# Performance work log

Measured on AMD Instinct MI355X. Metric: run time of the kernel, lower is better.

The kernel has to match this reference:

```python
import jax, jax.numpy as jnp
import numpy as np

H, C = 8, 32          # heads, out_channels per head (H*C = 256)
D = H * C
NEG_SLOPE = 0.2
SELF_LOOP_TYPE = 6    # num_edge_types - 1
EPS_LN = 1e-5
EPS_BN = 1e-5


def _gat_layer(x, src, dst, ea, et, Ws, Wd, a_s, a_d, We, ae, te, Wo, bo, b, lg, lb):
    N = x.shape[0]
    xs = (x @ Ws).reshape(N, H, C)   # lin_src -> x_j features
    xd = (x @ Wd).reshape(N, H, C)   # lin_dst -> x_i features
    # per-node attention logits (gathered per edge): alpha = <x_i, att_src> + <x_j, att_dst>
    a_i = jnp.einsum('nhc,hc->nh', xd, a_s)  # paired with x_i (dst)
    a_j = jnp.einsum('nhc,hc->nh', xs, a_d)  # paired with x_j (src)
    alpha = a_i[dst] + a_j[src]                                  # [E, H]
    ef = (ea @ We).reshape(-1, H, C)                              # lin_edge
    alpha = alpha + jnp.einsum('ehc,hc->eh', ef, ae)
    tf = te[et].reshape(-1, H, C)                                 # edge_type_emb
    alpha = alpha + jnp.einsum('ehc,hc->eh', tf, ae)
    alpha = jnp.where(alpha >= 0, alpha, NEG_SLOPE * alpha)       # leaky_relu
    # segment softmax over destination nodes (every node has a self loop)
    m = jax.ops.segment_max(alpha, dst, num_segments=N)
    e = jnp.exp(alpha - m[dst])
    s = jax.ops.segment_sum(e, dst, num_segments=N)
    alpha = e / (s[dst] + 1e-16)                                  # [E, H]
    # dropout is identity in eval mode
    msg = xs[src] * alpha[:, :, None]                             # [E, H, C]
    out = jax.ops.segment_sum(msg, dst, num_segments=N).reshape(N, D)
    out = out @ Wo + bo + b                                       # lin_out + bias
    mu = out.mean(-1, keepdims=True)
    var = out.var(-1, keepdims=True)
    out = (out - mu) / jnp.sqrt(var + EPS_LN) * lg + lb           # layer norm
    return out + x                                                # in_channels == H*C residual


def _bn_relu(x, g, bvec, relu=True):
    mu = x.mean(0)
    var = x.var(0)
    x = (x - mu) / jnp.sqrt(var + EPS_BN) * g + bvec
    return jnp.maximum(x, 0.0) if relu else x


def _forward(x, edge_index, edge_attr, edge_types,
             Ws1, Wd1, as1, ad1, We1, ae1, te1, Wo1, bo1, b1, lg1, lb1,
             Ws2, Wd2, as2, ad2, We2, ae2, te2, Wo2, bo2, b2, lg2, lb2,
             bng1, bnb1, bng2, bnb2):
    N = x.shape[0]
    loops = jnp.arange(N, dtype=edge_index.dtype)
    src = jnp.concatenate([edge_index[0], loops])
    dst = jnp.concatenate([edge_index[1], loops])
    ea = jnp.concatenate([edge_attr, jnp.ones((N, edge_attr.shape[1]), edge_attr.dtype)])
    et = jnp.concatenate([edge_types, jnp.full((N,), SELF_LOOP_TYPE, edge_types.dtype)])
    residual = x  # in_channels == out_channels -> identity projection
    out = _gat_layer(x, src, dst, ea, et, Ws1, Wd1, as1, ad1, We1, ae1, te1, Wo1, bo1, b1, lg1, lb1)
    out = _bn_relu(out, bng1, bnb1, relu=True)   # dropout identity in eval
    out = _gat_layer(out, src, dst, ea, et, Ws2, Wd2, as2, ad2, We2, ae2, te2, Wo2, bo2, b2, lg2, lb2)
    out = _bn_relu(out, bng2, bnb2, relu=False)
    return jnp.maximum(out + residual, 0.0)


def setup_inputs() -> dict:
    key = jax.random.key(0)
    ks = jax.random.split(key, 32)
    N, E, EDIM, NTYPES = 20000, 320000, 16, 7
    d = {}
    d['x'] = jax.random.normal(ks[0], (N, D), jnp.float32)
    d['edge_index'] = jax.random.randint(ks[1], (2, E), 0, N, jnp.int64)
    d['edge_attr'] = jax.random.normal(ks[2], (E, EDIM), jnp.float32)
    d['edge_types'] = jax.random.randint(ks[3], (E,), 0, NTYPES, jnp.int64)
    def glorot(k, shape):
        fan = shape[-2] + shape[-1] if len(shape) >= 2 else shape[-1] + 1
        return jax.random.uniform(k, shape, jnp.float32, -1.0, 1.0) * np.sqrt(6.0 / fan)
    i = 4
    for L in ('1', '2'):
        d['Ws' + L] = glorot(ks[i], (D, D)); i += 1
        d['Wd' + L] = glorot(ks[i], (D, D)); i += 1
        d['as' + L] = glorot(ks[i], (H, C)); i += 1
        d['ad' + L] = glorot(ks[i], (H, C)); i += 1
        d['We' + L] = glorot(ks[i], (EDIM, D)); i += 1
        d['ae' + L] = glorot(ks[i], (H, C)); i += 1
        d['te' + L] = glorot(ks[i], (NTYPES, D)); i += 1
        d['Wo' + L] = glorot(ks[i], (D, D)); i += 1
        d['bo' + L] = jnp.zeros((D,), jnp.float32)
        d['b' + L] = jnp.zeros((D,), jnp.float32)
        d['lg' + L] = jnp.ones((D,), jnp.float32)
        d['lb' + L] = jnp.zeros((D,), jnp.float32)
    d['bng1'] = jnp.ones((D,), jnp.float32); d['bnb1'] = jnp.zeros((D,), jnp.float32)
    d['bng2'] = jnp.ones((D,), jnp.float32); d['bnb2'] = jnp.zeros((D,), jnp.float32)
    return d


def reference(x, edge_index, edge_attr, edge_types,
              Ws1, Wd1, as1, ad1, We1, ae1, te1, Wo1, bo1, b1, lg1, lb1,
              Ws2, Wd2, as2, ad2, We2, ae2, te2, Wo2, bo2, b2, lg2, lb2,
              bng1, bnb1, bng2, bnb2):
    return _forward(x, edge_index, edge_attr, edge_types,
                    Ws1, Wd1, as1, ad1, We1, ae1, te1, Wo1, bo1, b1, lg1, lb1,
                    Ws2, Wd2, as2, ad2, We2, ae2, te2, Wo2, bo2, b2, lg2, lb2,
                    bng1, bnb1, bng2, bnb2)
```

## Files before the change

kernel.cpp:

```cpp
#include <hip/hip_runtime.h>

#define DD 256
#define HH 8
#define CC 32
#define DCACHE 128

typedef __attribute__((ext_vector_type(8))) short short8;
typedef __attribute__((ext_vector_type(4))) float f32x4;

static __device__ __forceinline__ unsigned short f2b(float f){
  unsigned u = __float_as_uint(f);
  u = u + 0x7FFFu + ((u >> 16) & 1u);
  return (unsigned short)(u >> 16);
}
static __device__ __forceinline__ float b2f(unsigned short s){
  return __uint_as_float(((unsigned)s) << 16);
}

static __device__ __forceinline__ void gload16(const void* g, void* l){
  using gpt = const __attribute__((address_space(1))) unsigned int*;
  using lpt = __attribute__((address_space(3))) unsigned int*;
  __builtin_amdgcn_global_load_lds((gpt)(unsigned long long)g, (lpt)(unsigned long long)l, 16, 0, 0);
}

__global__ void k_zero_i(int* p, int n){ int i=blockIdx.x*blockDim.x+threadIdx.x; if(i<n) p[i]=0; }

__global__ void k_count(const int* __restrict__ dstE, int E, int N, int* cnt){
  int e=blockIdx.x*blockDim.x+threadIdx.x;
  if(e<E+N){ int d=(e<E)? dstE[e] : (e-E); atomicAdd(&cnt[d],1); }
}

__global__ __launch_bounds__(1024) void k_scan(const int* __restrict__ cnt, int N, int* row_off, int* cursor){
  __shared__ int part[1024];
  int t=threadIdx.x;
  int chunk=(N+1023)>>10;
  int s=0;
  for(int j=0;j<chunk;j++){ int i=t*chunk+j; if(i<N) s+=cnt[i]; }
  part[t]=s; __syncthreads();
  for(int off=1; off<1024; off<<=1){
    int v=(t>=off)? part[t-off]:0;
    __syncthreads();
    part[t]+=v;
    __syncthreads();
  }
  int run=(t==0)?0:part[t-1];
  for(int j=0;j<chunk;j++){ int i=t*chunk+j; if(i<N){ row_off[i]=run; cursor[i]=run; run+=cnt[i]; } }
  if(t==1023) row_off[N]=part[1023];
}

__global__ void k_fill(const int* __restrict__ srcE, const int* __restrict__ dstE,
                       const float* __restrict__ ea, const int* __restrict__ et,
                       int E, int N, int* cursor,
                       int* esrc, int* etP, float* eaP){
  int e=blockIdx.x*blockDim.x+threadIdx.x;
  if(e>=E+N) return;
  int s,d,ty;
  float4 q0,q1,q2,q3;
  if(e<E){
    s=srcE[e]; d=dstE[e]; ty=et[e];
    q0=*(const float4*)&ea[(size_t)e*16+0];
    q1=*(const float4*)&ea[(size_t)e*16+4];
    q2=*(const float4*)&ea[(size_t)e*16+8];
    q3=*(const float4*)&ea[(size_t)e*16+12];
  }else{
    s=e-E; d=s; ty=6;
    q0=q1=q2=q3=make_float4(1.f,1.f,1.f,1.f);
  }
  int pos=atomicAdd(&cursor[d],1);
  esrc[pos]=s; etP[pos]=ty;
  float* o=&eaP[(size_t)pos*16];
  *(float4*)(o+0)=q0; *(float4*)(o+4)=q1; *(float4*)(o+8)=q2; *(float4*)(o+12)=q3;
}

__global__ void k_cvt_wT4(const float* __restrict__ W0, const float* __restrict__ W1,
                          const float* __restrict__ W2, const float* __restrict__ W3,
                          unsigned short* __restrict__ T0, unsigned short* __restrict__ T1,
                          unsigned short* __restrict__ T2, unsigned short* __restrict__ T3){
  int m=blockIdx.y, c=blockIdx.x, k=threadIdx.x;
  const float* W = (m==0)?W0:(m==1)?W1:(m==2)?W2:W3;
  unsigned short* T = (m==0)?T0:(m==1)?T1:(m==2)?T2:T3;
  T[(size_t)c*DD+k] = f2b(W[(size_t)k*DD+c]);
}

__global__ void k_pre2(const float* __restrict__ Wd1, const float* __restrict__ as1,
                       const float* __restrict__ We1, const float* __restrict__ ae1,
                       const float* __restrict__ te1,
                       const float* __restrict__ Wd2, const float* __restrict__ as2,
                       const float* __restrict__ We2, const float* __restrict__ ae2,
                       const float* __restrict__ te2,
                       float* wd_as1, float* v_e1, float* t_a1,
                       float* wd_as2, float* v_e2, float* t_a2){
  int L=blockIdx.x;
  const float* Wd=L?Wd2:Wd1; const float* as_=L?as2:as1;
  const float* We=L?We2:We1; const float* ae=L?ae2:ae1; const float* te=L?te2:te1;
  float* wd_as=L?wd_as2:wd_as1; float* v_e=L?v_e2:v_e1; float* t_a=L?t_a2:t_a1;
  int t=threadIdx.x;
  for(int idx=t; idx<DD*HH; idx+=256){
    int k=idx>>3, h=idx&7;
    const float* w=&Wd[k*DD+h*CC]; const float* a=&as_[h*CC];
    float s=0;
    #pragma unroll
    for(int c=0;c<CC;c++) s+=w[c]*a[c];
    wd_as[idx]=s;
  }
  for(int idx=t; idx<16*HH; idx+=256){
    int k=idx>>3, h=idx&7;
    const float* w=&We[k*DD+h*CC]; const float* a=&ae[h*CC];
    float s=0;
    #pragma unroll
    for(int c=0;c<CC;c++) s+=w[c]*a[c];
    v_e[idx]=s;
  }
  for(int idx=t; idx<7*HH; idx+=256){
    int k=idx>>3, h=idx&7;
    const float* w=&te[k*DD+h*CC]; const float* a=&ae[h*CC];
    float s=0;
    #pragma unroll
    for(int c=0;c<CC;c++) s+=w[c]*a[c];
    t_a[idx]=s;
  }
}

#define NB_BA 1024
__global__ __launch_bounds__(256) void k_cvt_x2(const float* __restrict__ xin, const float* __restrict__ wd_as,
                         unsigned short* __restrict__ xb, float* __restrict__ a_i, int N){
  int b=blockIdx.x, tid=threadIdx.x, wv=tid>>6, l=tid&63;
  int c0=4*l;
  float wa[4][8];
  #pragma unroll
  for(int j=0;j<4;j++)
    #pragma unroll
    for(int h=0;h<8;h++) wa[j][h]=wd_as[(c0+j)*8+h];
  for(int n=b*4+wv; n<N; n+=NB_BA*4){
    float4 v=*(const float4*)&xin[(size_t)n*DD+c0];
    ushort4 xo; xo.x=f2b(v.x); xo.y=f2b(v.y); xo.z=f2b(v.z); xo.w=f2b(v.w);
    *(ushort4*)&xb[(size_t)n*DD+c0]=xo;
    float ai[8];
    #pragma unroll
    for(int h=0;h<8;h++) ai[h]=v.x*wa[0][h]+v.y*wa[1][h]+v.z*wa[2][h]+v.w*wa[3][h];
    #pragma unroll
    for(int off=1;off<64;off<<=1){
      #pragma unroll
      for(int h=0;h<8;h++) ai[h]+=__shfl_xor(ai[h],off);
    }
    if(l==0){
      float4 A; A.x=ai[0];A.y=ai[1];A.z=ai[2];A.w=ai[3];
      float4 B; B.x=ai[4];B.y=ai[5];B.z=ai[6];B.w=ai[7];
      *(float4*)&a_i[(size_t)n*HH]=A;
      *(float4*)&a_i[(size_t)n*HH+4]=B;
    }
  }
}

template<bool AJ>
__global__ __launch_bounds__(256) void k_gemm1(const unsigned short* __restrict__ A,
                                               const unsigned short* __restrict__ Bt,
                                               const float* __restrict__ ad, float* __restrict__ a_j,
                                               unsigned short* __restrict__ Cout, int N){
  __shared__ char lds[2*12288];
  int tid=threadIdx.x;
  int w=tid>>6, l=tid&63;
  int row0=blockIdx.y*64, col0=blockIdx.x*128;

  int lr=l>>2;
  int kc=(l&3)^((l>>3)&3);
  const unsigned short* ga  = &A [(size_t)(row0+16*w+lr)*DD + kc*8];
  const unsigned short* gb0 = &Bt[(size_t)(col0+32*w+lr)*DD + kc*8];
  const unsigned short* gb1 = &Bt[(size_t)(col0+32*w+16+lr)*DD + kc*8];
  int laoff =      w*1024;
  int lboff0=4096+(32*w)*64;
  int lboff1=4096+(32*w+16)*64;

  int x15=l&15;
  int lp=x15*64 + ((l>>4)^((x15>>1)&3))*16;

  f32x4 acc[4][2];
  #pragma unroll
  for(int i=0;i<4;i++){ acc[i][0]=(f32x4)0.f; acc[i][1]=(f32x4)0.f; }

  gload16(ga,  lds+laoff);
  gload16(gb0, lds+lboff0);
  gload16(gb1, lds+lboff1);
  __syncthreads();
  int cur=0;
  for(int kt=0;kt<DD;kt+=32){
    int nxt=cur^1;
    if(kt+32<DD){
      gload16(ga +kt+32, lds+nxt*12288+laoff);
      gload16(gb0+kt+32, lds+nxt*12288+lboff0);
      gload16(gb1+kt+32, lds+nxt*12288+lboff1);
    }
    char* base=lds+cur*12288;
    short8 af[4], bf[2];
    #pragma unroll
    for(int mf=0;mf<4;mf++) af[mf]=*(short8*)(base + mf*1024 + lp);
    #pragma unroll
    for(int nf=0;nf<2;nf++) bf[nf]=*(short8*)(base + 4096 + (32*w+16*nf)*64 + lp);
    #pragma unroll
    for(int mf=0;mf<4;mf++)
      #pragma unroll
      for(int nf=0;nf<2;nf++)
        acc[mf][nf]=__builtin_amdgcn_mfma_f32_16x16x32_bf16(af[mf],bf[nf],acc[mf][nf],0,0,0);
    __syncthreads();
    cur=nxt;
  }

  int lcol=x15, lrow4=(l>>4)*4;
  float ad0=0.f, ad1=0.f;
  if(AJ){ ad0=ad[col0+32*w+lcol]; ad1=ad[col0+32*w+16+lcol]; }
  int head=(col0>>5)+w;
  #pragma unroll
  for(int mf=0;mf<4;mf++){
    #pragma unroll
    for(int nf=0;nf<2;nf++){
      int col=col0 + 32*w + 16*nf + lcol;
      #pragma unroll
      for(int rr=0;rr<4;rr++){
        int row=row0 + 16*mf + lrow4 + rr;
        if(row<N) Cout[(size_t)row*DD+col]=f2b(acc[mf][nf][rr]);
      }
    }
    if(AJ){
      #pragma unroll
      for(int rr=0;rr<4;rr++){
        float t=acc[mf][0][rr]*ad0 + acc[mf][1][rr]*ad1;
        t+=__shfl_xor(t,1); t+=__shfl_xor(t,2);
        t+=__shfl_xor(t,4); t+=__shfl_xor(t,8);
        int row=row0 + 16*mf + lrow4 + rr;
        if(x15==0 && row<N) a_j[(size_t)row*HH+head]=t;
      }
    }
  }
}

__global__ __launch_bounds__(256) void k_gemm_ln(const unsigned short* __restrict__ A,
                                                 const unsigned short* __restrict__ Bt,
                                                 const float* __restrict__ bo, const float* __restrict__ bvec,
                                                 const float* __restrict__ xin,
                                                 const float* __restrict__ lg, const float* __restrict__ lb,
                                                 float* __restrict__ hout,
                                                 float* __restrict__ psum, float* __restrict__ psq, int N){
  __shared__ char lds[2*18432];
  int tid=threadIdx.x;
  int w=tid>>6, l=tid&63;
  int row0=blockIdx.x*32;

  int lr=l>>2;
  int kc=(l&3)^((l>>3)&3);
  const unsigned short* ga = &A[(size_t)(row0+16*w+lr)*DD + kc*8];
  const unsigned short* gb0=&Bt[(size_t)(64*w   +lr)*DD + kc*8];
  const unsigned short* gb1=&Bt[(size_t)(64*w+16+lr)*DD + kc*8];
  const unsigned short* gb2=&Bt[(size_t)(64*w+32+lr)*DD + kc*8];
  const unsigned short* gb3=&Bt[(size_t)(64*w+48+lr)*DD + kc*8];
  int laoff =      w*1024;
  int lboff0=2048+(64*w   )*64;
  int lboff1=2048+(64*w+16)*64;
  int lboff2=2048+(64*w+32)*64;
  int lboff3=2048+(64*w+48)*64;

  int x15=l&15;
  int lp=x15*64 + ((l>>4)^((x15>>1)&3))*16;

  f32x4 acc[2][4];
  #pragma unroll
  for(int i=0;i<2;i++)
    #pragma unroll
    for(int j=0;j<4;j++) acc[i][j]=(f32x4)0.f;

  if(w<2) gload16(ga, lds+laoff);
  gload16(gb0, lds+lboff0);
  gload16(gb1, lds+lboff1);
  gload16(gb2, lds+lboff2);
  gload16(gb3, lds+lboff3);
  __syncthreads();
  int cur=0;
  for(int kt=0;kt<DD;kt+=32){
    int nxt=cur^1;
    if(kt+32<DD){
      char* nb=lds+nxt*18432;
      if(w<2) gload16(ga+kt+32, nb+laoff);
      gload16(gb0+kt+32, nb+lboff0);
      gload16(gb1+kt+32, nb+lboff1);
      gload16(gb2+kt+32, nb+lboff2);
      gload16(gb3+kt+32, nb+lboff3);
    }
    char* base=lds+cur*18432;
    short8 af[2], bf[4];
    #pragma unroll
    for(int mf=0;mf<2;mf++) af[mf]=*(short8*)(base + mf*1024 + lp);
    #pragma unroll
    for(int nf=0;nf<4;nf++) bf[nf]=*(short8*)(base + 2048 + (64*w+16*nf)*64 + lp);
    #pragma unroll
    for(int mf=0;mf<2;mf++)
      #pragma unroll
      for(int nf=0;nf<4;nf++)
        acc[mf][nf]=__builtin_amdgcn_mfma_f32_16x16x32_bf16(af[mf],bf[nf],acc[mf][nf],0,0,0);
    __syncthreads();
    cur=nxt;
  }

  int lrow4=(l>>4)*4;
  float lgv[4], lbv[4];
  #pragma unroll
  for(int nf=0;nf<4;nf++){
    int col=64*w+16*nf+x15;
    float badd=bo[col]+bvec[col];
    lgv[nf]=lg[col]; lbv[nf]=lb[col];
    #pragma unroll
    for(int mf=0;mf<2;mf++)
      #pragma unroll
      for(int rr=0;rr<4;rr++) acc[mf][nf][rr]+=badd;
  }
  __syncthreads();
  float* rs   =(float*)lds;
  float* rq   =(float*)(lds+512);
  float* mus  =(float*)(lds+1024);
  float* rstds=(float*)(lds+1152);
  #pragma unroll
  for(int mf=0;mf<2;mf++){
    #pragma unroll
    for(int rr=0;rr<4;rr++){
      float t=acc[mf][0][rr]+acc[mf][1][rr]+acc[mf][2][rr]+acc[mf][3][rr];
      float q=acc[mf][0][rr]*acc[mf][0][rr]+acc[mf][1][rr]*acc[mf][1][rr]
             +acc[mf][2][rr]*acc[mf][2][rr]+acc[mf][3][rr]*acc[mf][3][rr];
      t+=__shfl_xor(t,1); q+=__shfl_xor(q,1);
      t+=__shfl_xor(t,2); q+=__shfl_xor(q,2);
      t+=__shfl_xor(t,4); q+=__shfl_xor(q,4);
      t+=__shfl_xor(t,8); q+=__shfl_xor(q,8);
      if(x15==0){
        int row=16*mf+lrow4+rr;
        rs[w*32+row]=t; rq[w*32+row]=q;
      }
    }
  }
  __syncthreads();
  if(tid<32){
    float S=rs[tid]+rs[32+tid]+rs[64+tid]+rs[96+tid];
    float Q=rq[tid]+rq[32+tid]+rq[64+tid]+rq[96+tid];
    float mu=S*(1.f/DD);
    float var=Q*(1.f/DD)-mu*mu;
    mus[tid]=mu;
    rstds[tid]=rsqrtf(var+1e-5f);
  }
  __syncthreads();
  float cps[4]={0.f,0.f,0.f,0.f}, cqs[4]={0.f,0.f,0.f,0.f};
  #pragma unroll
  for(int mf=0;mf<2;mf++){
    #pragma unroll
    for(int rr=0;rr<4;rr++){
      int row=16*mf+lrow4+rr;
      int grow=row0+row;
      bool ok=(grow<N);
      float mu=mus[row], rstd=rstds[row];
      #pragma unroll
      for(int nf=0;nf<4;nf++){
        int col=64*w+16*nf+x15;
        float h=0.f;
        if(ok){
          h=(acc[mf][nf][rr]-mu)*rstd*lgv[nf]+lbv[nf]+xin[(size_t)grow*DD+col];
          hout[(size_t)grow*DD+col]=h;
        }
        cps[nf]+=h; cqs[nf]+=h*h;
      }
    }
  }
  #pragma unroll
  for(int nf=0;nf<4;nf++){
    cps[nf]+=__shfl_xor(cps[nf],16); cqs[nf]+=__shfl_xor(cqs[nf],16);
    cps[nf]+=__shfl_xor(cps[nf],32); cqs[nf]+=__shfl_xor(cqs[nf],32);
  }
  if(l<16){
    #pragma unroll
    for(int nf=0;nf<4;nf++){
      int col=64*w+16*nf+l;
      psum[(size_t)blockIdx.x*DD+col]=cps[nf];
      psq [(size_t)blockIdx.x*DD+col]=cqs[nf];
    }
  }
}

__global__ __launch_bounds__(256) void k_agg(const int* __restrict__ row_off,
                      const int* __restrict__ esrc, const int* __restrict__ etP,
                      const float* __restrict__ eaP,
                      const float* __restrict__ a_i, const float* __restrict__ a_j,
                      const float* __restrict__ v_e, const float* __restrict__ t_a,
                      const unsigned short* __restrict__ ysb, unsigned short* __restrict__ aggb, int N){
  __shared__ float cache[4][DCACHE][8];
  __shared__ int   scache[4][DCACHE];
  int wv=threadIdx.x>>6, l=threadIdx.x&63;
  int n=blockIdx.x*4+wv;
  if(n>=N) return;
  int beg=row_off[n], deg=row_off[n+1]-beg;
  int slotL=l>>3, headL=l&7;
  float veh[16];
  #pragma unroll
  for(int k=0;k<16;k++) veh[k]=v_e[k*8+headL];
  float aih=a_i[(size_t)n*HH+headL];
  float mx=-3e38f;
  for(int i=slotL;i<deg;i+=8){
    size_t pos=(size_t)(beg+i);
    int src=esrc[pos];
    int ty=etP[pos];
    float aj=a_j[(size_t)src*HH+headL];
    const float* eap=&eaP[pos*16];
    float4 q0=*(const float4*)(eap+0);
    float4 q1=*(const float4*)(eap+4);
    float4 q2=*(const float4*)(eap+8);
    float4 q3=*(const float4*)(eap+12);
    float v=aih+aj+t_a[ty*8+headL];
    v+=q0.x*veh[0]+q0.y*veh[1]+q0.z*veh[2]+q0.w*veh[3];
    v+=q1.x*veh[4]+q1.y*veh[5]+q1.z*veh[6]+q1.w*veh[7];
    v+=q2.x*veh[8]+q2.y*veh[9]+q2.z*veh[10]+q2.w*veh[11];
    v+=q3.x*veh[12]+q3.y*veh[13]+q3.z*veh[14]+q3.w*veh[15];
    v=(v>=0.f)? v : 0.2f*v;
    if(i<DCACHE){
      cache[wv][i][headL]=v;
      if(headL==0) scache[wv][i]=src;
    }
    mx=fmaxf(mx,v);
  }
  mx=fmaxf(mx,__shfl_xor(mx,8));
  mx=fmaxf(mx,__shfl_xor(mx,16));
  mx=fmaxf(mx,__shfl_xor(mx,32));
  int ghead=l>>3;
  float m_g=__shfl(mx,ghead);
  float ssum=0.f, acc0=0.f, acc1=0.f, acc2=0.f, acc3=0.f;
  for(int base=0;base<deg;base+=8){
    int cnt=min(8,deg-base);
    #pragma unroll
    for(int u=0;u<8;u++){
      if(u<cnt){
        int i=base+u;
        float vv; int si;
        if(i<DCACHE){
          vv=cache[wv][i][ghead];
          si=scache[wv][i];
        }else{
          size_t pos=(size_t)(beg+i);
          si=esrc[pos];
          int ty=etP[pos];
          float v=a_i[(size_t)n*HH+ghead]+a_j[(size_t)si*HH+ghead]+t_a[ty*8+ghead];
          const float* eap=&eaP[pos*16];
          #pragma unroll
          for(int k=0;k<16;k++) v+=eap[k]*v_e[k*8+ghead];
          vv=(v>=0.f)? v : 0.2f*v;
        }
        float wgt=__expf(vv-m_g);
        ssum+=wgt;
        ushort4 y=*(const ushort4*)&ysb[(size_t)si*DD+4*l];
        acc0+=wgt*b2f(y.x); acc1+=wgt*b2f(y.y); acc2+=wgt*b2f(y.z); acc3+=wgt*b2f(y.w);
      }
    }
  }
  float inv=1.f/(ssum+1e-16f);
  ushort4 o;
  o.x=f2b(acc0*inv); o.y=f2b(acc1*inv); o.z=f2b(acc2*inv); o.w=f2b(acc3*inv);
  *(ushort4*)&aggb[(size_t)n*DD+4*l]=o;
}

__global__ __launch_bounds__(256) void k_bnfin(const float* __restrict__ psum, const float* __restrict__ psq,
                        const float* __restrict__ g, const float* __restrict__ b,
                        float* scale, float* shift, int N, int nb){
  __shared__ float rs[256], rq[256];
  int c=blockIdx.x, tid=threadIdx.x;
  float s=0.f,q=0.f;
  for(int i=tid;i<nb;i+=256){ s+=psum[(size_t)i*DD+c]; q+=psq[(size_t)i*DD+c]; }
  rs[tid]=s; rq[tid]=q;
  __syncthreads();
  #pragma unroll
  for(int off=128;off>0;off>>=1){
    if(tid<off){ rs[tid]+=rs[tid+off]; rq[tid]+=rq[tid+off]; }
    __syncthreads();
  }
  if(tid==0){
    float inv=1.f/(float)N;
    float mu=rs[0]*inv;
    float var=rq[0]*inv - mu*mu;
    float sc=g[c]*rsqrtf(var+1e-5f);
    scale[c]=sc;
    shift[c]=b[c]-mu*sc;
  }
}

template<bool RES, bool CVT>
__global__ __launch_bounds__(256) void k_bnapply(const float* __restrict__ hm, const float* __restrict__ scale,
                          const float* __restrict__ shift, const float* __restrict__ res,
                          float* __restrict__ outp, unsigned short* __restrict__ xb,
                          const float* __restrict__ wd_as, float* __restrict__ a_i, int N){
  int b=blockIdx.x, tid=threadIdx.x, wv=tid>>6, l=tid&63;
  int c0=4*l;
  float4 sc=*(const float4*)&scale[c0];
  float4 sh=*(const float4*)&shift[c0];
  float wa[4][8];
  if(CVT){
    #pragma unroll
    for(int j=0;j<4;j++)
      #pragma unroll
      for(int h=0;h<8;h++) wa[j][h]=wd_as[(c0+j)*8+h];
  }
  for(int n=b*4+wv; n<N; n+=NB_BA*4){
    float4 v=*(const float4*)&hm[(size_t)n*DD+c0];
    v.x=v.x*sc.x+sh.x; v.y=v.y*sc.y+sh.y; v.z=v.z*sc.z+sh.z; v.w=v.w*sc.w+sh.w;
    if(RES){
      float4 rr=*(const float4*)&res[(size_t)n*DD+c0];
      v.x+=rr.x; v.y+=rr.y; v.z+=rr.z; v.w+=rr.w;
    }
    v.x=fmaxf(v.x,0.f); v.y=fmaxf(v.y,0.f); v.z=fmaxf(v.z,0.f); v.w=fmaxf(v.w,0.f);
    *(float4*)&outp[(size_t)n*DD+c0]=v;
    if(CVT){
      ushort4 xo; xo.x=f2b(v.x); xo.y=f2b(v.y); xo.z=f2b(v.z); xo.w=f2b(v.w);
      *(ushort4*)&xb[(size_t)n*DD+c0]=xo;
      float ai[8];
      #pragma unroll
      for(int h=0;h<8;h++) ai[h]=v.x*wa[0][h]+v.y*wa[1][h]+v.z*wa[2][h]+v.w*wa[3][h];
      #pragma unroll
      for(int off=1;off<64;off<<=1){
        #pragma unroll
        for(int h=0;h<8;h++) ai[h]+=__shfl_xor(ai[h],off);
      }
      if(l==0){
        float4 A; A.x=ai[0];A.y=ai[1];A.z=ai[2];A.w=ai[3];
        float4 B; B.x=ai[4];B.y=ai[5];B.z=ai[6];B.w=ai[7];
        *(float4*)&a_i[(size_t)n*HH]=A;
        *(float4*)&a_i[(size_t)n*HH+4]=B;
      }
    }
  }
}

extern "C" void kernel_launch(void* const* d_in, const int* in_sizes, int n_in,
                              void* d_out, int out_size, void* d_ws, size_t ws_size,
                              hipStream_t stream) {
  const float* x  = (const float*)d_in[0];
  const int*   ei = (const int*)d_in[1];
  const float* ea = (const float*)d_in[2];
  const int*   et = (const int*)d_in[3];
  int N = in_sizes[0]/DD;
  int E = in_sizes[3];
  int Etot = E+N;
  const int* srcE = ei;
  const int* dstE = ei + E;

  const float* Ws1=(const float*)d_in[4];  const float* Wd1=(const float*)d_in[5];
  const float* as1=(const float*)d_in[6];  const float* ad1=(const float*)d_in[7];
  const float* We1=(const float*)d_in[8];  const float* ae1=(const float*)d_in[9];
  const float* te1=(const float*)d_in[10]; const float* Wo1=(const float*)d_in[11];
  const float* bo1=(const float*)d_in[12]; const float* b1 =(const float*)d_in[13];
  const float* lg1=(const float*)d_in[14]; const float* lb1=(const float*)d_in[15];
  const float* Ws2=(const float*)d_in[16]; const float* Wd2=(const float*)d_in[17];
  const float* as2=(const float*)d_in[18]; const float* ad2=(const float*)d_in[19];
  const float* We2=(const float*)d_in[20]; const float* ae2=(const float*)d_in[21];
  const float* te2=(const float*)d_in[22]; const float* Wo2=(const float*)d_in[23];
  const float* bo2=(const float*)d_in[24]; const float* b2 =(const float*)d_in[25];
  const float* lg2=(const float*)d_in[26]; const float* lb2=(const float*)d_in[27];
  const float* bng1=(const float*)d_in[28]; const float* bnb1=(const float*)d_in[29];
  const float* bng2=(const float*)d_in[30]; const float* bnb2=(const float*)d_in[31];

  char* p=(char*)d_ws;
  auto alloc=[&](size_t bytes)->void*{ void* r=(void*)p; p+=(bytes+255)&~(size_t)255; return r; };
  unsigned short* xb   =(unsigned short*)alloc((size_t)N*DD*2);
  unsigned short* ysb  =(unsigned short*)alloc((size_t)N*DD*2);
  unsigned short* aggb =(unsigned short*)alloc((size_t)N*DD*2);
  float* eaP   =(float*)alloc((size_t)Etot*16*4);
  int*   etP   =(int*)alloc((size_t)Etot*4);
  float* xout1 =(float*)alloc((size_t)N*DD*4);
  float* a_i   =(float*)alloc((size_t)N*HH*4);
  float* a_j   =(float*)alloc((size_t)N*HH*4);
  float* wd_as1=(float*)alloc(DD*HH*4);
  float* v_e1  =(float*)alloc(16*HH*4);
  float* t_a1  =(float*)alloc(7*HH*4);
  float* wd_as2=(float*)alloc(DD*HH*4);
  float* v_e2  =(float*)alloc(16*HH*4);
  float* t_a2  =(float*)alloc(7*HH*4);
  int nbLN=(N+31)/32;
  float* psum  =(float*)alloc((size_t)nbLN*DD*4);
  float* psq   =(float*)alloc((size_t)nbLN*DD*4);
  float* scl   =(float*)alloc(256*4);
  float* shf   =(float*)alloc(256*4);
  unsigned short* Wsb1T=(unsigned short*)alloc((size_t)DD*DD*2);
  unsigned short* Wob1T=(unsigned short*)alloc((size_t)DD*DD*2);
  unsigned short* Wsb2T=(unsigned short*)alloc((size_t)DD*DD*2);
  unsigned short* Wob2T=(unsigned short*)alloc((size_t)DD*DD*2);
  int* cnt     =(int*)alloc((size_t)N*4);
  int* row_off =(int*)alloc((size_t)(N+1)*4);
  int* cursor  =(int*)alloc((size_t)N*4);
  int* esrc    =(int*)alloc((size_t)Etot*4);
  float* hbuf  =(float*)d_out;

  dim3 gg(2,(N+63)/64);
  int aggGrid=(N+3)/4;

  k_zero_i<<<(N+255)/256,256,0,stream>>>(cnt,N);
  k_count<<<(Etot+255)/256,256,0,stream>>>(dstE,E,N,cnt);
  k_scan<<<1,1024,0,stream>>>(cnt,N,row_off,cursor);
  k_fill<<<(Etot+255)/256,256,0,stream>>>(srcE,dstE,ea,et,E,N,cursor,esrc,etP,eaP);
  k_cvt_wT4<<<dim3(DD,4),DD,0,stream>>>(Ws1,Wo1,Ws2,Wo2,Wsb1T,Wob1T,Wsb2T,Wob2T);
  k_pre2<<<2,256,0,stream>>>(Wd1,as1,We1,ae1,te1,Wd2,as2,We2,ae2,te2,
                             wd_as1,v_e1,t_a1,wd_as2,v_e2,t_a2);

  k_cvt_x2<<<NB_BA,256,0,stream>>>(x,wd_as1,xb,a_i,N);
  k_gemm1<true><<<gg,256,0,stream>>>(xb,Wsb1T,ad1,a_j,ysb,N);
  k_agg<<<aggGrid,256,0,stream>>>(row_off,esrc,etP,eaP,a_i,a_j,v_e1,t_a1,ysb,aggb,N);
  k_gemm_ln<<<nbLN,256,0,stream>>>(aggb,Wob1T,bo1,b1,x,lg1,lb1,hbuf,psum,psq,N);
  k_bnfin<<<DD,256,0,stream>>>(psum,psq,bng1,bnb1,scl,shf,N,nbLN);
  k_bnapply<false,true><<<NB_BA,256,0,stream>>>(hbuf,scl,shf,nullptr,xout1,xb,wd_as2,a_i,N);

  k_gemm1<true><<<gg,256,0,stream>>>(xb,Wsb2T,ad2,a_j,ysb,N);
  k_agg<<<aggGrid,256,0,stream>>>(row_off,esrc,etP,eaP,a_i,a_j,v_e2,t_a2,ysb,aggb,N);
  k_gemm_ln<<<nbLN,256,0,stream>>>(aggb,Wob2T,bo2,b2,xout1,lg2,lb2,hbuf,psum,psq,N);
  k_bnfin<<<DD,256,0,stream>>>(psum,psq,bng2,bnb2,scl,shf,N,nbLN);
  k_bnapply<true,false><<<NB_BA,256,0,stream>>>(hbuf,scl,shf,x,(float*)d_out,nullptr,nullptr,nullptr,N);
}
```

Baseline: 318.4 us.

## Fuse attention scoring and aggregation into single-pass online softmax in k_agg

Replaces the two-pass aggregation (first compute logits and max into an LDS cache, then reread and accumulate) with one pass over edges in chunks of 8. Each chunk computes its logits, reduces a chunk max across lanes and rescales the running sum and accumulators online. Logits and source indices reach the other lanes through shuffles instead of shared memory. This removes the LDS cache and its fallback recompute for high-degree nodes, at the cost of extra exp rescaling and shuffles per chunk.

```diff
diff --git a/kernel.cpp b/kernel.cpp
--- a/kernel.cpp
+++ b/kernel.cpp
@@ -3,7 +3,6 @@
 #define DD 256
 #define HH 8
 #define CC 32
-#define DCACHE 128
 
 typedef __attribute__((ext_vector_type(8))) short short8;
 typedef __attribute__((ext_vector_type(4))) float f32x4;
@@ -385,67 +384,56 @@
                       const float* __restrict__ a_i, const float* __restrict__ a_j,
                       const float* __restrict__ v_e, const float* __restrict__ t_a,
                       const unsigned short* __restrict__ ysb, unsigned short* __restrict__ aggb, int N){
-  __shared__ float cache[4][DCACHE][8];
-  __shared__ int   scache[4][DCACHE];
   int wv=threadIdx.x>>6, l=threadIdx.x&63;
   int n=blockIdx.x*4+wv;
   if(n>=N) return;
   int beg=row_off[n], deg=row_off[n+1]-beg;
   int slotL=l>>3, headL=l&7;
+  int ghead=l>>3;
   float veh[16];
   #pragma unroll
   for(int k=0;k<16;k++) veh[k]=v_e[k*8+headL];
   float aih=a_i[(size_t)n*HH+headL];
-  float mx=-3e38f;
-  for(int i=slotL;i<deg;i+=8){
-    size_t pos=(size_t)(beg+i);
+  float m=-3e38f, ssum=0.f, acc0=0.f, acc1=0.f, acc2=0.f, acc3=0.f;
+  for(int base=0;base<deg;base+=8){
+    int i=base+slotL;
+    bool ok=(i<deg);
+    int ic=ok?i:(deg-1);
+    size_t pos=(size_t)(beg+ic);
     int src=esrc[pos];
-    int ty=etP[pos];
-    float aj=a_j[(size_t)src*HH+headL];
-    const float* eap=&eaP[pos*16];
-    float4 q0=*(const float4*)(eap+0);
-    float4 q1=*(const float4*)(eap+4);
-    float4 q2=*(const float4*)(eap+8);
-    float4 q3=*(const float4*)(eap+12);
-    float v=aih+aj+t_a[ty*8+headL];
-    v+=q0.x*veh[0]+q0.y*veh[1]+q0.z*veh[2]+q0.w*veh[3];
-    v+=q1.x*veh[4]+q1.y*veh[5]+q1.z*veh[6]+q1.w*veh[7];
-    v+=q2.x*veh[8]+q2.y*veh[9]+q2.z*veh[10]+q2.w*veh[11];
-    v+=q3.x*veh[12]+q3.y*veh[13]+q3.z*veh[14]+q3.w*veh[15];
-    v=(v>=0.f)? v : 0.2f*v;
-    if(i<DCACHE){
-      cache[wv][i][headL]=v;
-      if(headL==0) scache[wv][i]=src;
-    }
-    mx=fmaxf(mx,v);
-  }
-  mx=fmaxf(mx,__shfl_xor(mx,8));
-  mx=fmaxf(mx,__shfl_xor(mx,16));
-  mx=fmaxf(mx,__shfl_xor(mx,32));
-  int ghead=l>>3;
-  float m_g=__shfl(mx,ghead);
-  float ssum=0.f, acc0=0.f, acc1=0.f, acc2=0.f, acc3=0.f;
-  for(int base=0;base<deg;base+=8){
+    float v=-3e38f;
+    {
+      int ty=etP[pos];
+      float aj=a_j[(size_t)src*HH+headL];
+      const float* eap=&eaP[pos*16];
+      float4 q0=*(const float4*)(eap+0);
+      float4 q1=*(const float4*)(eap+4);
+      float4 q2=*(const float4*)(eap+8);
+      float4 q3=*(const float4*)(eap+12);
+      float t=aih+aj+t_a[ty*8+headL];
+      t+=q0.x*veh[0]+q0.y*veh[1]+q0.z*veh[2]+q0.w*veh[3];
+      t+=q1.x*veh[4]+q1.y*veh[5]+q1.z*veh[6]+q1.w*veh[7];
+      t+=q2.x*veh[8]+q2.y*veh[9]+q2.z*veh[10]+q2.w*veh[11];
+      t+=q3.x*veh[12]+q3.y*veh[13]+q3.z*veh[14]+q3.w*veh[15];
+      t=(t>=0.f)? t : 0.2f*t;
+      if(ok) v=t;
+    }
+    float cm=v;
+    cm=fmaxf(cm,__shfl_xor(cm,8));
+    cm=fmaxf(cm,__shfl_xor(cm,16));
+    cm=fmaxf(cm,__shfl_xor(cm,32));
+    float cmg=__shfl(cm,ghead);
+    float mnew=fmaxf(m,cmg);
+    float f=__expf(m-mnew);
+    ssum*=f; acc0*=f; acc1*=f; acc2*=f; acc3*=f;
+    m=mnew;
     int cnt=min(8,deg-base);
     #pragma unroll
     for(int u=0;u<8;u++){
       if(u<cnt){
-        int i=base+u;
-        float vv; int si;
-        if(i<DCACHE){
-          vv=cache[wv][i][ghead];
-          si=scache[wv][i];
-        }else{
-          size_t pos=(size_t)(beg+i);
-          si=esrc[pos];
-          int ty=etP[pos];
-          float v=a_i[(size_t)n*HH+ghead]+a_j[(size_t)si*HH+ghead]+t_a[ty*8+ghead];
-          const float* eap=&eaP[pos*16];
-          #pragma unroll
-          for(int k=0;k<16;k++) v+=eap[k]*v_e[k*8+ghead];
-          vv=(v>=0.f)? v : 0.2f*v;
-        }
-        float wgt=__expf(vv-m_g);
+        float vu=__shfl(v,(u<<3)|ghead);
+        int   si=__shfl(src,(u<<3));
+        float wgt=__expf(vu-m);
         ssum+=wgt;
         ushort4 y=*(const ushort4*)&ysb[(size_t)si*DD+4*l];
         acc0+=wgt*b2f(y.x); acc1+=wgt*b2f(y.y); acc2+=wgt*b2f(y.z); acc3+=wgt*b2f(y.w);
```

After: 319.0 us. Within noise of the previous version (+0.2%).
